# Performance work log

Hardware: AMD Instinct MI355X
Metric: run time of the kernel (lower is better)

Reference implementation:

```python
import jax, jax.numpy as jnp
import numpy as np

B, S, H, F_IN = 256, 128, 512, 1


def _lstm_step(h, c, x, Wih, Whh, b):
    # PyTorch LSTM gate order: i, f, g, o
    gates = x @ Wih.T + h @ Whh.T + b  # (B, 4H)
    i, f, g, o = jnp.split(gates, 4, axis=-1)
    c = jax.nn.sigmoid(f) * c + jax.nn.sigmoid(i) * jnp.tanh(g)
    h = jax.nn.sigmoid(o) * jnp.tanh(c)
    return h, c


def setup_inputs() -> dict:
    key = jax.random.key(0)
    ks = jax.random.split(key, 18)
    p = lambda k, shape: (jax.random.normal(k, shape, dtype=jnp.float32) * 0.05)
    return {
        "input_seq": jax.random.normal(ks[0], (B, S, F_IN), dtype=jnp.float32),
        # encoder: embedding Linear(F_IN -> H) + LSTM(H -> H)
        "We_e": p(ks[1], (H, F_IN)), "be_e": p(ks[2], (H,)),
        "Wih_e": p(ks[3], (4 * H, H)), "Whh_e": p(ks[4], (4 * H, H)), "b_e": p(ks[5], (4 * H,)),
        # decoder: embedding Linear(F_IN -> H) + LSTMCell(H -> H)
        "We_d": p(ks[6], (H, F_IN)), "be_d": p(ks[7], (H,)),
        "Wih_d": p(ks[8], (4 * H, H)), "Whh_d": p(ks[9], (4 * H, H)), "b_d": p(ks[10], (4 * H,)),
        # additive attention: W_1, W_2 (H->H), v (H->1)
        "W1": p(ks[11], (H, H)), "b1": p(ks[12], (H,)),
        "W2": p(ks[13], (H, H)), "b2": p(ks[14], (H,)),
        "v": p(ks[15], (1, H)), "bv": p(ks[16], (1,)),
    }


def reference(input_seq, We_e, be_e, Wih_e, Whh_e, b_e,
              We_d, be_d, Wih_d, Whh_d, b_d,
              W1, b1, W2, b2, v, bv):
    # ---- encoder: embed then LSTM over the sequence ----
    emb = input_seq @ We_e.T + be_e  # (B, S, H)

    def enc_step(carry, x_t):
        h, c = carry
        h, c = _lstm_step(h, c, x_t, Wih_e, Whh_e, b_e)
        return (h, c), h

    h0 = jnp.zeros((B, H), dtype=input_seq.dtype)
    (h, c), enc_h = jax.lax.scan(enc_step, (h0, h0), jnp.swapaxes(emb, 0, 1))
    encoder_output = jnp.swapaxes(enc_h, 0, 1)  # (B, S, H)

    # W_1(encoder_output) is loop-invariant; hoist it (same math as the
    # original, which redundantly recomputes it every step).
    w1enc = encoder_output @ W1.T + b1  # (B, S, H)

    # ---- decoder: per-step LSTMCell + additive attention ----
    def dec_step(carry, _):
        hd, cd, x_in = carry
        e = x_in @ We_d.T + be_d  # (B, H)
        hd, cd = _lstm_step(hd, cd, e, Wih_d, Whh_d, b_d)
        q = hd @ W2.T + b2  # (B, H)
        u = jnp.squeeze(jnp.tanh(w1enc + q[:, None, :]) @ v.T + bv, -1)  # (B, S)
        att = jax.nn.log_softmax(u, axis=1)
        idx = jnp.argmax(att, axis=1)  # pointer (B,)
        # next decoder input = pointed-to input symbol
        x_next = jnp.take_along_axis(input_seq[:, :, 0], idx[:, None], axis=1)  # (B, 1)
        return (hd, cd, x_next), (att, idx)

    x0 = jnp.zeros((B, 1), dtype=input_seq.dtype)
    _, (scores, ptrs) = jax.lax.scan(dec_step, (h, c, x0), None, length=S)
    pointers_scores = jnp.swapaxes(scores, 0, 1)  # (B, S, S) log-probs
    pointers = jnp.swapaxes(ptrs, 0, 1)  # (B, S) int
    return pointers_scores, pointers
```

## Files before the change

### kernel.cpp

```cpp
#include <hip/hip_runtime.h>
#include <hip/hip_fp16.h>

#define Bn 256
#define Sn 128
#define Hn 512
#define G4 2048
#define NBLK 512
#define NTHR 512
#define HSTR 516
#define LOG2E 1.4426950408889634f

typedef float f4v __attribute__((ext_vector_type(4)));

__device__ __forceinline__ float sigf(float x){
    float e = expf(-fabsf(x));
    float d = 1.f + e;
    return x >= 0.f ? 1.f/d : e/d;
}
__device__ __forceinline__ float ftanh(float x){
    float e = __builtin_amdgcn_exp2f(-2.f * LOG2E * fabsf(x));
    float t = (1.f - e) * __builtin_amdgcn_rcpf(1.f + e);
    return copysignf(t, x);
}

__device__ __forceinline__ float cload(const float* p){
    return __hip_atomic_load((float*)p, __ATOMIC_RELAXED, __HIP_MEMORY_SCOPE_AGENT);
}
__device__ __forceinline__ void cstore(float* p, float v){
    __hip_atomic_store(p, v, __ATOMIC_RELAXED, __HIP_MEMORY_SCOPE_AGENT);
}
__device__ __forceinline__ f4v vload4(const float* p){
    return *(volatile const f4v*)p;
}

__device__ __forceinline__ void gbar(unsigned* cnt, unsigned k){
    __syncthreads();
    if (threadIdx.x == 0) {
        __hip_atomic_fetch_add(cnt, 1u, __ATOMIC_RELAXED, __HIP_MEMORY_SCOPE_AGENT);
        while (__hip_atomic_load(cnt, __ATOMIC_RELAXED, __HIP_MEMORY_SCOPE_AGENT) < 16u*k)
            __builtin_amdgcn_s_sleep(1);
        asm volatile("" ::: "memory");
    }
    __syncthreads();
}
__device__ __forceinline__ void gbar_sys(unsigned* cnt, unsigned k){
    __syncthreads();
    if (threadIdx.x == 0) {
        __hip_atomic_fetch_add(cnt, 1u, __ATOMIC_RELEASE, __HIP_MEMORY_SCOPE_AGENT);
        while (__hip_atomic_load(cnt, __ATOMIC_RELAXED, __HIP_MEMORY_SCOPE_AGENT) < 16u*k)
            __builtin_amdgcn_s_sleep(1);
        (void)__hip_atomic_load(cnt, __ATOMIC_ACQUIRE, __HIP_MEMORY_SCOPE_AGENT);
    }
    __syncthreads();
}

__global__ void precompute_kernel(
    const float* __restrict__ Wih_e, const float* __restrict__ We_e,
    const float* __restrict__ be_e,  const float* __restrict__ b_e,
    const float* __restrict__ Wih_d, const float* __restrict__ We_d,
    const float* __restrict__ be_d,  const float* __restrict__ b_d,
    float* __restrict__ p1, float* __restrict__ p0,
    float* __restrict__ r1, float* __restrict__ r0)
{
    int j = blockIdx.x*blockDim.x + threadIdx.x;
    bool dec = j >= G4;
    int jj = dec ? j - G4 : j;
    const float* Wih = dec ? Wih_d : Wih_e;
    const float* We  = dec ? We_d  : We_e;
    const float* be  = dec ? be_d  : be_e;
    const float* bb  = dec ? b_d   : b_e;
    float s1 = 0.f, s0 = 0.f;
    for (int k = 0; k < Hn; ++k) {
        float w = Wih[jj*Hn + k];
        s1 += w * We[k];
        s0 += w * be[k];
    }
    s0 += bb[jj];
    if (dec) { r1[jj] = s1; r0[jj] = s0; }
    else     { p1[jj] = s1; p0[jj] = s0; }
}

__global__ __launch_bounds__(NTHR, 4) void ptrnet_kernel(
    const float* __restrict__ xseq,
    const float* __restrict__ Whh_e, const float* __restrict__ Whh_d,
    const float* __restrict__ W1, const float* __restrict__ b1,
    const float* __restrict__ W2, const float* __restrict__ b2,
    const float* __restrict__ vv,
    const float* __restrict__ p1, const float* __restrict__ p0,
    const float* __restrict__ r1, const float* __restrict__ r0,
    float* __restrict__ hb0, float* __restrict__ hb1,
    float* __restrict__ cbuf, float* __restrict__ qbuf,
    float* __restrict__ x_in, float* __restrict__ w1enc,
    unsigned* __restrict__ barb,
    float* __restrict__ out_scores, float* __restrict__ out_ptr)
{
    __shared__ float smem[8*HSTR + 256*5 + 64];
    float* hs  = smem;
    float* red = smem + 8*HSTR;
    float* qs  = smem;
    float* us  = smem + Hn;
    float* rr  = smem + Hn + Sn + 8;

    const int blk = blockIdx.x;
    const int tid = threadIdx.x;
    const int bt  = blk >> 4, grp = blk & 15;
    const int b0  = bt << 3;
    const int tb  = tid & 7;
    const int hh  = (tid >> 3) & 31;
    const int ks  = tid >> 8;
    const int hg  = (grp << 5) + hh;
    const int kofs = ks << 8;
    const int ridx = (tid & 255) * 5;
    unsigned* gcnt = barb + bt*64;
    unsigned bk = 0;
    float* hprev = hb0;
    float* hnext = hb1;

    const int l64 = tid & 63;
    const int kb = l64 << 3;
    float vreg[8];
    #pragma unroll
    for (int j = 0; j < 8; ++j) vreg[j] = vv[kb+j];

#define STAGE_H(SRC) do { \
    for (int i_ = tid; i_ < 1024; i_ += NTHR) { \
        int r_ = i_ >> 7, c4_ = (i_ & 127) << 2; \
        *(f4v*)(hs + r_*HSTR + c4_) = vload4((SRC) + (size_t)(b0+r_)*Hn + c4_); \
    } __syncthreads(); } while(0)

    for (int t = 0; t <= Sn; ++t) {
        STAGE_H(hprev);
        float a0=0.f,a1=0.f,a2=0.f,a3=0.f,a4=0.f;
        {
            const float* hrow = hs + tb*HSTR + kofs;
            const float* w0 = Whh_e + (size_t)hg*Hn          + kofs;
            const float* w1r= Whh_e + (size_t)(Hn+hg)*Hn     + kofs;
            const float* w2r= Whh_e + (size_t)(2*Hn+hg)*Hn   + kofs;
            const float* w3r= Whh_e + (size_t)(3*Hn+hg)*Hn   + kofs;
            const float* w4r= W1    + (size_t)hg*Hn          + kofs;
            for (int i = 0; i < 256; i += 4) {
                float4 hv = *(const float4*)(hrow + i);
                float4 x0 = *(const float4*)(w0 + i);
                float4 x1 = *(const float4*)(w1r + i);
                float4 x2 = *(const float4*)(w2r + i);
                float4 x3 = *(const float4*)(w3r + i);
                float4 x4 = *(const float4*)(w4r + i);
                a0 += hv.x*x0.x + hv.y*x0.y + hv.z*x0.z + hv.w*x0.w;
                a1 += hv.x*x1.x + hv.y*x1.y + hv.z*x1.z + hv.w*x1.w;
                a2 += hv.x*x2.x + hv.y*x2.y + hv.z*x2.z + hv.w*x2.w;
                a3 += hv.x*x3.x + hv.y*x3.y + hv.z*x3.z + hv.w*x3.w;
                a4 += hv.x*x4.x + hv.y*x4.y + hv.z*x4.z + hv.w*x4.w;
            }
        }
        if (ks) {
            float* rp = red + ridx;
            rp[0]=a0; rp[1]=a1; rp[2]=a2; rp[3]=a3; rp[4]=a4;
        }
        __syncthreads();
        if (!ks) {
            const float* rp = red + ridx;
            a0+=rp[0]; a1+=rp[1]; a2+=rp[2]; a3+=rp[3]; a4+=rp[4];
            size_t off = (size_t)(b0+tb)*Hn + hg;
            if (t < Sn) {
                float xv = xseq[(b0+tb)*Sn + t];
                float gi = a0 + xv*p1[hg]      + p0[hg];
                float gf = a1 + xv*p1[Hn+hg]   + p0[Hn+hg];
                float gg = a2 + xv*p1[2*Hn+hg] + p0[2*Hn+hg];
                float go = a3 + xv*p1[3*Hn+hg] + p0[3*Hn+hg];
                float cn = sigf(gf)*cbuf[off] + sigf(gi)*tanhf(gg);
                float hn = sigf(go)*tanhf(cn);
                cbuf[off] = cn;
                cstore(hnext + off, hn);
            }
            if (t > 0)
                w1enc[((size_t)(b0+tb)*Sn + (t-1))*Hn + hg] = a4 + b1[hg];
        }
        ++bk;
        if (t == Sn) gbar_sys(gcnt, bk);
        else         gbar(gcnt, bk);
        if (t < Sn) { float* tp = hprev; hprev = hnext; hnext = tp; }
    }

    for (int t = 0; t < Sn; ++t) {
        STAGE_H(hprev);
        float a0=0.f,a1=0.f,a2=0.f,a3=0.f;
        {
            const float* hrow = hs + tb*HSTR + kofs;
            const float* w0 = Whh_d + (size_t)hg*Hn        + kofs;
            const float* w1r= Whh_d + (size_t)(Hn+hg)*Hn   + kofs;
            const float* w2r= Whh_d + (size_t)(2*Hn+hg)*Hn + kofs;
            const float* w3r= Whh_d + (size_t)(3*Hn+hg)*Hn + kofs;
            for (int i = 0; i < 256; i += 4) {
                float4 hv = *(const float4*)(hrow + i);
                float4 x0 = *(const float4*)(w0 + i);
                float4 x1 = *(const float4*)(w1r + i);
                float4 x2 = *(const float4*)(w2r + i);
                float4 x3 = *(const float4*)(w3r + i);
                a0 += hv.x*x0.x + hv.y*x0.y + hv.z*x0.z + hv.w*x0.w;
                a1 += hv.x*x1.x + hv.y*x1.y + hv.z*x1.z + hv.w*x1.w;
                a2 += hv.x*x2.x + hv.y*x2.y + hv.z*x2.z + hv.w*x2.w;
                a3 += hv.x*x3.x + hv.y*x3.y + hv.z*x3.z + hv.w*x3.w;
            }
        }
        if (ks) {
            float* rp = red + ridx;
            rp[0]=a0; rp[1]=a1; rp[2]=a2; rp[3]=a3;
        }
        __syncthreads();
        if (!ks) {
            const float* rp = red + ridx;
            a0+=rp[0]; a1+=rp[1]; a2+=rp[2]; a3+=rp[3];
            size_t off = (size_t)(b0+tb)*Hn + hg;
            float xv = cload(x_in + b0 + tb);
            float gi = a0 + xv*r1[hg]      + r0[hg];
            float gf = a1 + xv*r1[Hn+hg]   + r0[Hn+hg];
            float gg = a2 + xv*r1[2*Hn+hg] + r0[2*Hn+hg];
            float go = a3 + xv*r1[3*Hn+hg] + r0[3*Hn+hg];
            float cn = sigf(gf)*cbuf[off] + sigf(gi)*tanhf(gg);
            float hn = sigf(go)*tanhf(cn);
            cbuf[off] = cn;
            cstore(hnext + off, hn);
        }
        ++bk; gbar(gcnt, bk);
        { float* tp = hprev; hprev = hnext; hnext = tp; }

        STAGE_H(hprev);
        float qa = 0.f;
        {
            const float* hrow = hs + tb*HSTR + kofs;
            const float* wq = W2 + (size_t)hg*Hn + kofs;
            for (int i = 0; i < 256; i += 4) {
                float4 hv = *(const float4*)(hrow + i);
                float4 wv = *(const float4*)(wq + i);
                qa += hv.x*wv.x + hv.y*wv.y + hv.z*wv.z + hv.w*wv.w;
            }
        }
        if (ks) red[tid - 256] = qa;
        __syncthreads();
        if (!ks) {
            qa += red[tid];
            cstore(qbuf + (size_t)(b0+tb)*Hn + hg, qa + b2[hg]);
        }
        ++bk; gbar(gcnt, bk);

        if (grp < 8) {
            const int b = b0 + grp;
            if (tid < 128) {
                f4v q4 = vload4(qbuf + (size_t)b*Hn + (tid << 2));
                *(f4v*)(qs + (tid << 2)) = q4;
            }
            __syncthreads();
            const int wv2 = tid >> 6;
            float qreg[8];
            #pragma unroll
            for (int j = 0; j < 8; ++j) qreg[j] = qs[kb+j];
            #pragma unroll
            for (int si = 0; si < 16; ++si) {
                const int s = (wv2 << 4) + si;
                const float* wr = w1enc + ((size_t)b*Sn + s)*Hn + kb;
                f4v w0 = *(const f4v*)wr;
                f4v w1v = *(const f4v*)(wr + 4);
                float a = 0.f;
                a += vreg[0]*ftanh(w0[0] + qreg[0]);
                a += vreg[1]*ftanh(w0[1] + qreg[1]);
                a += vreg[2]*ftanh(w0[2] + qreg[2]);
                a += vreg[3]*ftanh(w0[3] + qreg[3]);
                a += vreg[4]*ftanh(w1v[0] + qreg[4]);
                a += vreg[5]*ftanh(w1v[1] + qreg[5]);
                a += vreg[6]*ftanh(w1v[2] + qreg[6]);
                a += vreg[7]*ftanh(w1v[3] + qreg[7]);
                a += __shfl_xor(a, 1);  a += __shfl_xor(a, 2);  a += __shfl_xor(a, 4);
                a += __shfl_xor(a, 8);  a += __shfl_xor(a, 16); a += __shfl_xor(a, 32);
                if (l64 == 0) us[s] = a;
            }
            __syncthreads();
            if (tid < 64) {
                float av = us[tid], c2 = us[tid+64];
                float mv; int mi;
                if (c2 > av) { mv = c2; mi = tid+64; } else { mv = av; mi = tid; }
                #pragma unroll
                for (int off2 = 1; off2 < 64; off2 <<= 1) {
                    float ov = __shfl_xor(mv, off2);
                    int   oi = __shfl_xor(mi, off2);
                    if (ov > mv || (ov == mv && oi < mi)) { mv = ov; mi = oi; }
                }
                float es = expf(av - mv) + expf(c2 - mv);
                #pragma unroll
                for (int off2 = 1; off2 < 64; off2 <<= 1) es += __shfl_xor(es, off2);
                if (tid == 0) {
                    rr[0] = mv; rr[1] = logf(es);
                    out_ptr[b*Sn + t] = (float)mi;
                    cstore(x_in + b, xseq[b*Sn + mi]);
                }
            }
            __syncthreads();
            if (tid < Sn)
                out_scores[((size_t)b*Sn + t)*Sn + tid] = us[tid] - rr[0] - rr[1];
        }
        if (t < Sn-1) { ++bk; gbar(gcnt, bk); }
    }
#undef STAGE_H
}

extern "C" void kernel_launch(void* const* d_in, const int* in_sizes, int n_in,
                              void* d_out, int out_size, void* d_ws, size_t ws_size,
                              hipStream_t stream)
{
    const float* input_seq = (const float*)d_in[0];
    const float* We_e = (const float*)d_in[1],  *be_e = (const float*)d_in[2];
    const float* Wih_e = (const float*)d_in[3], *Whh_e = (const float*)d_in[4];
    const float* b_e = (const float*)d_in[5];
    const float* We_d = (const float*)d_in[6],  *be_d = (const float*)d_in[7];
    const float* Wih_d = (const float*)d_in[8], *Whh_d = (const float*)d_in[9];
    const float* b_d = (const float*)d_in[10];
    const float* W1 = (const float*)d_in[11], *b1 = (const float*)d_in[12];
    const float* W2 = (const float*)d_in[13], *b2 = (const float*)d_in[14];
    const float* v  = (const float*)d_in[15];

    float* ws = (float*)d_ws;
    size_t o = 0;
    float* hb0  = ws + o; o += Bn*Hn;
    float* hb1  = ws + o; o += Bn*Hn;
    float* cbuf = ws + o; o += Bn*Hn;
    float* qbuf = ws + o; o += Bn*Hn;
    float* p1   = ws + o; o += G4;
    float* p0   = ws + o; o += G4;
    float* r1   = ws + o; o += G4;
    float* r0   = ws + o; o += G4;
    float* x_in = ws + o; o += 256;
    unsigned* barb = (unsigned*)(ws + o); o += 2048;
    float* w1enc = ws + o;

    hipMemsetAsync(hb0,  0, Bn*Hn*sizeof(float), stream);
    hipMemsetAsync(cbuf, 0, Bn*Hn*sizeof(float), stream);
    hipMemsetAsync(x_in, 0, (256+2048)*sizeof(float), stream);

    precompute_kernel<<<dim3(16), 256, 0, stream>>>(Wih_e, We_e, be_e, b_e,
                                                    Wih_d, We_d, be_d, b_d,
                                                    p1, p0, r1, r0);

    ptrnet_kernel<<<dim3(NBLK), dim3(NTHR), 0, stream>>>(
        input_seq, Whh_e, Whh_d, W1, b1, W2, b2, v,
        p1, p0, r1, r0, hb0, hb1, cbuf, qbuf, x_in, w1enc, barb,
        (float*)d_out, (float*)d_out + (size_t)Bn*Sn*Sn);
}
```

Baseline: 14.17 ms.

## Use 256 blocks of 1024 threads with 16-batch tiles and slot-based group barriers

Halves the block count and doubles threads per block, so each block now covers 16 batch rows instead of 8. Each weight row it streams therefore serves twice as many batch rows, and every block now owns one batch for the attention step. The group barrier changes from a shared atomic counter to per-block slots that a wavefront polls with a ballot, which removes atomic contention on the counter. Costs are a lower launch-bounds occupancy (1024 threads per block), more LDS per block, and the weight loads in the hot loop now spread over fewer CUs.

```diff
diff --git a/kernel.cpp b/kernel.cpp
--- a/kernel.cpp
+++ b/kernel.cpp
@@ -5,8 +5,8 @@
 #define Sn 128
 #define Hn 512
 #define G4 2048
-#define NBLK 512
-#define NTHR 512
+#define NBLK 256
+#define NTHR 1024
 #define HSTR 516
 #define LOG2E 1.4426950408889634f
 
@@ -33,21 +33,29 @@
     return *(volatile const f4v*)p;
 }
 
-__device__ __forceinline__ void gbar(unsigned* cnt, unsigned k){
+__device__ __forceinline__ void gbar(unsigned* slots, unsigned k, int grp){
     __syncthreads();
-    if (threadIdx.x == 0) {
-        __hip_atomic_fetch_add(cnt, 1u, __ATOMIC_RELAXED, __HIP_MEMORY_SCOPE_AGENT);
-        while (__hip_atomic_load(cnt, __ATOMIC_RELAXED, __HIP_MEMORY_SCOPE_AGENT) < 16u*k)
+    if (threadIdx.x < 64) {
+        if (threadIdx.x == 0)
+            __hip_atomic_store(slots + grp, k, __ATOMIC_RELAXED, __HIP_MEMORY_SCOPE_AGENT);
+        unsigned v = (threadIdx.x < 16)
+            ? __hip_atomic_load(slots + threadIdx.x, __ATOMIC_RELAXED, __HIP_MEMORY_SCOPE_AGENT)
+            : k;
+        while (__ballot(v < k)) {
             __builtin_amdgcn_s_sleep(1);
+            v = (threadIdx.x < 16)
+                ? __hip_atomic_load(slots + threadIdx.x, __ATOMIC_RELAXED, __HIP_MEMORY_SCOPE_AGENT)
+                : k;
+        }
         asm volatile("" ::: "memory");
     }
     __syncthreads();
 }
-__device__ __forceinline__ void gbar_sys(unsigned* cnt, unsigned k){
+__device__ __forceinline__ void gbar_sys(unsigned* cnt){
     __syncthreads();
     if (threadIdx.x == 0) {
         __hip_atomic_fetch_add(cnt, 1u, __ATOMIC_RELEASE, __HIP_MEMORY_SCOPE_AGENT);
-        while (__hip_atomic_load(cnt, __ATOMIC_RELAXED, __HIP_MEMORY_SCOPE_AGENT) < 16u*k)
+        while (__hip_atomic_load(cnt, __ATOMIC_RELAXED, __HIP_MEMORY_SCOPE_AGENT) < 16u)
             __builtin_amdgcn_s_sleep(1);
         (void)__hip_atomic_load(cnt, __ATOMIC_ACQUIRE, __HIP_MEMORY_SCOPE_AGENT);
     }
@@ -94,9 +102,9 @@
     unsigned* __restrict__ barb,
     float* __restrict__ out_scores, float* __restrict__ out_ptr)
 {
-    __shared__ float smem[8*HSTR + 256*5 + 64];
+    __shared__ float smem[16*HSTR + 512*5 + 16];
     float* hs  = smem;
-    float* red = smem + 8*HSTR;
+    float* red = smem + 16*HSTR;
     float* qs  = smem;
     float* us  = smem + Hn;
     float* rr  = smem + Hn + Sn + 8;
@@ -104,14 +112,14 @@
     const int blk = blockIdx.x;
     const int tid = threadIdx.x;
     const int bt  = blk >> 4, grp = blk & 15;
-    const int b0  = bt << 3;
-    const int tb  = tid & 7;
-    const int hh  = (tid >> 3) & 31;
-    const int ks  = tid >> 8;
+    const int b0  = bt << 4;
+    const int tb  = tid & 15;
+    const int hh  = (tid >> 4) & 31;
+    const int ks  = tid >> 9;
     const int hg  = (grp << 5) + hh;
     const int kofs = ks << 8;
-    const int ridx = (tid & 255) * 5;
-    unsigned* gcnt = barb + bt*64;
+    unsigned* slots  = barb + bt*64;
+    unsigned* syscnt = barb + 1024 + bt*64;
     unsigned bk = 0;
     float* hprev = hb0;
     float* hnext = hb1;
@@ -123,8 +131,8 @@
     for (int j = 0; j < 8; ++j) vreg[j] = vv[kb+j];
 
 #define STAGE_H(SRC) do { \
-    for (int i_ = tid; i_ < 1024; i_ += NTHR) { \
-        int r_ = i_ >> 7, c4_ = (i_ & 127) << 2; \
+    for (int i_ = tid; i_ < 16*128; i_ += NTHR) { \
+        int r_ = i_ >> 7; int c4_ = (i_ & 127) << 2; \
         *(f4v*)(hs + r_*HSTR + c4_) = vload4((SRC) + (size_t)(b0+r_)*Hn + c4_); \
     } __syncthreads(); } while(0)
 
@@ -153,12 +161,12 @@
             }
         }
         if (ks) {
-            float* rp = red + ridx;
+            float* rp = red + (size_t)(tid - 512)*5;
             rp[0]=a0; rp[1]=a1; rp[2]=a2; rp[3]=a3; rp[4]=a4;
         }
         __syncthreads();
         if (!ks) {
-            const float* rp = red + ridx;
+            const float* rp = red + (size_t)tid*5;
             a0+=rp[0]; a1+=rp[1]; a2+=rp[2]; a3+=rp[3]; a4+=rp[4];
             size_t off = (size_t)(b0+tb)*Hn + hg;
             if (t < Sn) {
@@ -175,9 +183,8 @@
             if (t > 0)
                 w1enc[((size_t)(b0+tb)*Sn + (t-1))*Hn + hg] = a4 + b1[hg];
         }
-        ++bk;
-        if (t == Sn) gbar_sys(gcnt, bk);
-        else         gbar(gcnt, bk);
+        if (t == Sn) gbar_sys(syscnt);
+        else         { ++bk; gbar(slots, bk, grp); }
         if (t < Sn) { float* tp = hprev; hprev = hnext; hnext = tp; }
     }
 
@@ -203,12 +210,12 @@
             }
         }
         if (ks) {
-            float* rp = red + ridx;
+            float* rp = red + (size_t)(tid - 512)*4;
             rp[0]=a0; rp[1]=a1; rp[2]=a2; rp[3]=a3;
         }
         __syncthreads();
         if (!ks) {
-            const float* rp = red + ridx;
+            const float* rp = red + (size_t)tid*4;
             a0+=rp[0]; a1+=rp[1]; a2+=rp[2]; a3+=rp[3];
             size_t off = (size_t)(b0+tb)*Hn + hg;
             float xv = cload(x_in + b0 + tb);
@@ -221,7 +228,7 @@
             cbuf[off] = cn;
             cstore(hnext + off, hn);
         }
-        ++bk; gbar(gcnt, bk);
+        ++bk; gbar(slots, bk, grp);
         { float* tp = hprev; hprev = hnext; hnext = tp; }
 
         STAGE_H(hprev);
@@ -235,69 +242,64 @@
                 qa += hv.x*wv.x + hv.y*wv.y + hv.z*wv.z + hv.w*wv.w;
             }
         }
-        if (ks) red[tid - 256] = qa;
-        __syncthreads();
-        if (!ks) {
-            qa += red[tid];
-            cstore(qbuf + (size_t)(b0+tb)*Hn + hg, qa + b2[hg]);
-        }
-        ++bk; gbar(gcnt, bk);
-
-        if (grp < 8) {
-            const int b = b0 + grp;
-            if (tid < 128) {
-                f4v q4 = vload4(qbuf + (size_t)b*Hn + (tid << 2));
-                *(f4v*)(qs + (tid << 2)) = q4;
-            }
-            __syncthreads();
-            const int wv2 = tid >> 6;
-            float qreg[8];
+        if (ks) red[tid - 512] = qa;
+        __syncthreads();
+        if (!ks) cstore(qbuf + (size_t)(b0+tb)*Hn + hg, qa + red[tid] + b2[hg]);
+        ++bk; gbar(slots, bk, grp);
+
+        const int b = blk;
+        if (tid < 128) {
+            f4v q4 = vload4(qbuf + (size_t)b*Hn + (tid << 2));
+            *(f4v*)(qs + (tid << 2)) = q4;
+        }
+        __syncthreads();
+        const int wv2 = tid >> 6;
+        float qreg[8];
+        #pragma unroll
+        for (int j = 0; j < 8; ++j) qreg[j] = qs[kb+j];
+        #pragma unroll
+        for (int si = 0; si < 8; ++si) {
+            const int s = (wv2 << 3) + si;
+            const float* wr = w1enc + ((size_t)b*Sn + s)*Hn + kb;
+            f4v w0 = *(const f4v*)wr;
+            f4v w1v = *(const f4v*)(wr + 4);
+            float a = 0.f;
+            a += vreg[0]*ftanh(w0[0] + qreg[0]);
+            a += vreg[1]*ftanh(w0[1] + qreg[1]);
+            a += vreg[2]*ftanh(w0[2] + qreg[2]);
+            a += vreg[3]*ftanh(w0[3] + qreg[3]);
+            a += vreg[4]*ftanh(w1v[0] + qreg[4]);
+            a += vreg[5]*ftanh(w1v[1] + qreg[5]);
+            a += vreg[6]*ftanh(w1v[2] + qreg[6]);
+            a += vreg[7]*ftanh(w1v[3] + qreg[7]);
+            a += __shfl_xor(a, 1);  a += __shfl_xor(a, 2);  a += __shfl_xor(a, 4);
+            a += __shfl_xor(a, 8);  a += __shfl_xor(a, 16); a += __shfl_xor(a, 32);
+            if (l64 == 0) us[s] = a;
+        }
+        __syncthreads();
+        if (tid < 64) {
+            float av = us[tid], c2 = us[tid+64];
+            float mv; int mi;
+            if (c2 > av) { mv = c2; mi = tid+64; } else { mv = av; mi = tid; }
             #pragma unroll
-            for (int j = 0; j < 8; ++j) qreg[j] = qs[kb+j];
+            for (int off2 = 1; off2 < 64; off2 <<= 1) {
+                float ov = __shfl_xor(mv, off2);
+                int   oi = __shfl_xor(mi, off2);
+                if (ov > mv || (ov == mv && oi < mi)) { mv = ov; mi = oi; }
+            }
+            float es = expf(av - mv) + expf(c2 - mv);
             #pragma unroll
-            for (int si = 0; si < 16; ++si) {
-                const int s = (wv2 << 4) + si;
-                const float* wr = w1enc + ((size_t)b*Sn + s)*Hn + kb;
-                f4v w0 = *(const f4v*)wr;
-                f4v w1v = *(const f4v*)(wr + 4);
-                float a = 0.f;
-                a += vreg[0]*ftanh(w0[0] + qreg[0]);
-                a += vreg[1]*ftanh(w0[1] + qreg[1]);
-                a += vreg[2]*ftanh(w0[2] + qreg[2]);
-                a += vreg[3]*ftanh(w0[3] + qreg[3]);
-                a += vreg[4]*ftanh(w1v[0] + qreg[4]);
-                a += vreg[5]*ftanh(w1v[1] + qreg[5]);
-                a += vreg[6]*ftanh(w1v[2] + qreg[6]);
-                a += vreg[7]*ftanh(w1v[3] + qreg[7]);
-                a += __shfl_xor(a, 1);  a += __shfl_xor(a, 2);  a += __shfl_xor(a, 4);
-                a += __shfl_xor(a, 8);  a += __shfl_xor(a, 16); a += __shfl_xor(a, 32);
-                if (l64 == 0) us[s] = a;
-            }
-            __syncthreads();
-            if (tid < 64) {
-                float av = us[tid], c2 = us[tid+64];
-                float mv; int mi;
-                if (c2 > av) { mv = c2; mi = tid+64; } else { mv = av; mi = tid; }
-                #pragma unroll
-                for (int off2 = 1; off2 < 64; off2 <<= 1) {
-                    float ov = __shfl_xor(mv, off2);
-                    int   oi = __shfl_xor(mi, off2);
-                    if (ov > mv || (ov == mv && oi < mi)) { mv = ov; mi = oi; }
-                }
-                float es = expf(av - mv) + expf(c2 - mv);
-                #pragma unroll
-                for (int off2 = 1; off2 < 64; off2 <<= 1) es += __shfl_xor(es, off2);
-                if (tid == 0) {
-                    rr[0] = mv; rr[1] = logf(es);
-                    out_ptr[b*Sn + t] = (float)mi;
-                    cstore(x_in + b, xseq[b*Sn + mi]);
-                }
-            }
-            __syncthreads();
-            if (tid < Sn)
-                out_scores[((size_t)b*Sn + t)*Sn + tid] = us[tid] - rr[0] - rr[1];
-        }
-        if (t < Sn-1) { ++bk; gbar(gcnt, bk); }
+            for (int off2 = 1; off2 < 64; off2 <<= 1) es += __shfl_xor(es, off2);
+            if (tid == 0) {
+                rr[0] = mv; rr[1] = logf(es);
+                out_ptr[b*Sn + t] = (float)mi;
+                cstore(x_in + b, xseq[b*Sn + mi]);
+            }
+        }
+        __syncthreads();
+        if (tid < Sn)
+            out_scores[((size_t)b*Sn + t)*Sn + tid] = us[tid] - rr[0] - rr[1];
+        if (t < Sn-1) { ++bk; gbar(slots, bk, grp); }
     }
 #undef STAGE_H
 }
```

Measured after the change: 12.94 ms. -8.7%, faster.
